# Kernel tuning notes

Measured on AMD Instinct MI355X. Metric: run time of the kernel, lower is better.

## Reference

```python
import jax, jax.numpy as jnp
import numpy as np
import math

B, N, D, O, H = 2, 3072, 64, 64, 4

def setup_inputs() -> dict:
    key = jax.random.key(0)
    ks = jax.random.split(key, 8)
    x = jax.random.normal(ks[0], (B, N, D), dtype=jnp.float32)
    edge_index = jax.random.randint(ks[1], (B, N, N), 0, 2, dtype=jnp.int32)
    s = 1.0 / math.sqrt(D)
    Wv = jax.random.uniform(ks[2], (H, D, O), jnp.float32, -s, s)
    bv = jax.random.uniform(ks[3], (H, O), jnp.float32, -s, s)
    Wq = jax.random.uniform(ks[4], (H, D, O), jnp.float32, -s, s)
    bq = jax.random.uniform(ks[5], (H, O), jnp.float32, -s, s)
    Wk = jax.random.uniform(ks[6], (H, D, O), jnp.float32, -s, s)
    bk = jax.random.uniform(ks[7], (H, O), jnp.float32, -s, s)
    return {"x": x, "edge_index": edge_index, "Wv": Wv, "bv": bv,
            "Wq": Wq, "bq": bq, "Wk": Wk, "bk": bk}

def reference(x, edge_index, Wv, bv, Wq, bq, Wk, bk):
    # x: [B,N,D]; edge_index: dense {0,1} adjacency [B,N,N]
    dk = jnp.asarray(math.sqrt(x.shape[-1]), x.dtype)
    v = jnp.einsum('bnd,hdo->bhno', x, Wv) + bv[None, :, None, :]
    q = jnp.einsum('bnd,hdo->bhno', x, Wq) + bq[None, :, None, :]
    k = jnp.einsum('bnd,hdo->bhno', x, Wk) + bk[None, :, None, :]
    scores = jnp.einsum('bhno,bhmo->bhnm', q, k) / dk        # [B,H,N,N]
    scores = jax.nn.leaky_relu(scores, 0.2)
    mask = (-1e10) * (1.0 - edge_index.astype(scores.dtype))  # [B,N,N]
    scores = scores + mask[:, None, :, :]
    prop = jax.nn.softmax(scores, axis=-1)
    # dropout on v omitted (inference mode: identity)
    feats = jnp.einsum('bhnm,bhmo->bhno', prop, v)            # [B,H,N,O]
    out = jnp.mean(feats, axis=1)                             # [B,N,O]
    return jax.nn.leaky_relu(out, 0.2)
```

## Files before the change

### kernel.cpp

```cpp
#include <hip/hip_runtime.h>
#include <hip/hip_bf16.h>
#include <cstdint>

#define Bc 2
#define Nc 3072
#define Hc 4
#define NW32 96
#define TILEB 8192
#define KSC 4
#define TPS (NW32/KSC)

typedef __bf16    bf16x8 __attribute__((ext_vector_type(8)));
typedef _Float16  f16x8  __attribute__((ext_vector_type(8)));
typedef _Float16  f16x4  __attribute__((ext_vector_type(4)));
typedef float     f32x16 __attribute__((ext_vector_type(16)));

#define QSCALE 0.18033688f

static __device__ __forceinline__ f32x16 mfma32bf(bf16x8 a, bf16x8 b, f32x16 c) {
    return __builtin_amdgcn_mfma_f32_32x32x16_bf16(a, b, c, 0, 0, 0);
}
static __device__ __forceinline__ f32x16 mfma32h(f16x8 a, f16x8 b, f32x16 c) {
    return __builtin_amdgcn_mfma_f32_32x32x16_f16(a, b, c, 0, 0, 0);
}
static __device__ __forceinline__ uint32_t pkrtz(float lo, float hi) {
    uint32_t w;
    asm("v_cvt_pkrtz_f16_f32 %0, %1, %2" : "=v"(w) : "v"(lo), "v"(hi));
    return w;
}

static __device__ __forceinline__ void softmax_pack(const f32x16& sc, uint32_t mwh,
                                                    uint32_t W8[8])
{
    #pragma unroll
    for (int i = 0; i < 8; ++i) {
        const int bp0 = (2*i & 3) + 8*(2*i >> 2);
        float s0 = sc[2*i], s1 = sc[2*i + 1];
        float a0 = fmaxf(s0, 0.2f*s0);
        float a1 = fmaxf(s1, 0.2f*s1);
        float e0, e1;
        asm("v_exp_f32 %0, %1" : "=v"(e0) : "v"(a0));
        asm("v_exp_f32 %0, %1" : "=v"(e1) : "v"(a1));
        uint32_t pk = pkrtz(e0, e1);
        uint32_t m0 = (uint32_t)__builtin_amdgcn_sbfe((int)mwh, bp0, 1);
        uint32_t m1 = (uint32_t)__builtin_amdgcn_sbfe((int)mwh, bp0 + 1, 1);
        uint32_t sel = (m0 & 0x0000ffffu) | (m1 & 0xffff0000u);
        W8[i] = pk & sel;
    }
}

static __device__ __forceinline__ void assemble_pa(uint32_t W8[8], f16x8& pa0, f16x8& pa1)
{
    uint32_t a0 = W8[0], a2 = W8[2], a1 = W8[1], a3 = W8[3];
    uint32_t b0 = W8[4], b2 = W8[6], b1 = W8[5], b3 = W8[7];
    asm("v_permlane32_swap_b32 %0, %1" : "+v"(a0), "+v"(a2));
    asm("v_permlane32_swap_b32 %0, %1" : "+v"(a1), "+v"(a3));
    asm("v_permlane32_swap_b32 %0, %1" : "+v"(b0), "+v"(b2));
    asm("v_permlane32_swap_b32 %0, %1" : "+v"(b1), "+v"(b3));
    union { uint32_t u[4]; f16x8 v; } u0, u1;
    u0.u[0] = a0; u0.u[1] = a1; u0.u[2] = a2; u0.u[3] = a3;
    u1.u[0] = b0; u1.u[1] = b1; u1.u[2] = b2; u1.u[3] = b3;
    pa0 = u0.v; pa1 = u1.v;
}

static __device__ __forceinline__ void load_subtile(const char* gt, int hi, int l31,
                                                    f16x8 (&K)[4], f16x8 (&V)[4])
{
    #pragma unroll
    for (int kk = 0; kk < 4; ++kk)
        K[kk] = *(const f16x8*)(gt + ((kk*2 + hi) << 9) + (l31 << 4));
    #pragma unroll
    for (int i = 0; i < 4; ++i) {
        const int kkp = i >> 1, ot = i & 1;
        V[i] = *(const f16x8*)(gt + 4096 + ((kkp*2 + hi) << 10) + ((ot*32 + l31) << 4));
    }
}

static __device__ __forceinline__ void compute_subtile(
    const f16x8 (&K)[4], const f16x8 (&V)[4], uint32_t mw, int hi,
    const f16x8 (&qf)[4], const f32x16& fzero, const f16x8& ones,
    f32x16& acc0, f32x16& acc1, f32x16& acc2)
{
    f32x16 sc;
    __builtin_amdgcn_s_setprio(1);
    sc = mfma32h(K[0], qf[0], fzero);
    sc = mfma32h(K[1], qf[1], sc);
    sc = mfma32h(K[2], qf[2], sc);
    sc = mfma32h(K[3], qf[3], sc);
    __builtin_amdgcn_s_setprio(0);

    uint32_t W8[8];
    softmax_pack(sc, mw >> (hi*4), W8);
    f16x8 pa0, pa1;
    assemble_pa(W8, pa0, pa1);

    __builtin_amdgcn_s_setprio(1);
    acc2 = mfma32h(pa0, ones, acc2);
    acc2 = mfma32h(pa1, ones, acc2);
    acc0 = mfma32h(pa0, V[0], acc0);
    acc1 = mfma32h(pa0, V[1], acc1);
    acc0 = mfma32h(pa1, V[2], acc0);
    acc1 = mfma32h(pa1, V[3], acc1);
    __builtin_amdgcn_s_setprio(0);
}

__global__ void preppack_kernel(const float* __restrict__ Wq, const float* __restrict__ Wk,
                                const float* __restrict__ Wv,
                                const float* __restrict__ bq, const float* __restrict__ bk,
                                const float* __restrict__ bv,
                                const int* __restrict__ edge,
                                __bf16* __restrict__ Wbh, __bf16* __restrict__ Wbl,
                                float* __restrict__ Bs, uint32_t* __restrict__ pmT)
{
    if (blockIdx.x < 192) {
        int i = blockIdx.x*256 + threadIdx.x;
        int d = i & 63, o = (i >> 6) & 63, h = (i >> 12) & 3, p = i >> 14;
        const float* W = (p == 0) ? Wq : (p == 1) ? Wk : Wv;
        float scale = (p == 0) ? QSCALE : 1.0f;
        float val = W[(h*64 + d)*64 + o] * scale;
        int idx = (((p*Hc + h)*64 + o) << 6) + d;
        __bf16 hi = (__bf16)val;
        Wbh[idx] = hi;
        Wbl[idx] = (__bf16)(val - (float)hi);
        if (i < 3*Hc*64) {
            int pp = i / (Hc*64), rest = i % (Hc*64);
            const float* B = (pp == 0) ? bq : (pp == 1) ? bk : bv;
            Bs[i] = B[rest] * ((pp == 0) ? QSCALE : 1.0f);
        }
    } else {
        int gw = (blockIdx.x - 192)*4 + (threadIdx.x >> 6);
        int lane = threadIdx.x & 63;
        int ng = gw % 48; gw /= 48;
        int w  = gw % NW32; gw /= NW32;
        int b  = gw;
        int n = ng*64 + lane;
        const uint4* ep = (const uint4*)(edge + ((size_t)b*Nc + n)*Nc + w*32);
        uint32_t word = 0;
        #pragma unroll
        for (int i = 0; i < 8; ++i) {
            uint4 e = ep[i];
            word |= (e.x ? 1u : 0u) << (4*i);
            word |= (e.y ? 1u : 0u) << (4*i + 1);
            word |= (e.z ? 1u : 0u) << (4*i + 2);
            word |= (e.w ? 1u : 0u) << (4*i + 3);
        }
        pmT[((size_t)b*NW32 + w)*Nc + n] = word;
    }
}

__global__ __launch_bounds__(256) void qkv_mfma(
    const float* __restrict__ x,
    const __bf16* __restrict__ Wbh, const __bf16* __restrict__ Wbl,
    const float* __restrict__ Bs,
    _Float16* __restrict__ Qf, _Float16* __restrict__ Kf,
    _Float16* __restrict__ KVimg)
{
    const int lane = threadIdx.x & 63, w = threadIdx.x >> 6;
    const int l31 = lane & 31, hi = lane >> 5;
    int t = blockIdx.x;
    int nt = t % 48; t /= 48;
    int b  = t & 1;  t >>= 1;
    int p  = t % 3;
    int h  = t / 3;
    const int r0 = (w >> 1)*32, c0 = (w & 1)*32, n0 = nt*64;

    bf16x8 xh[4], xl[4], wh[4], wl[4];
    #pragma unroll
    for (int kk = 0; kk < 4; ++kk) {
        size_t xoff = (((size_t)(b*Nc + n0 + r0 + l31)) << 6) + kk*16 + hi*8;
        float4 f0 = *(const float4*)(x + xoff);
        float4 f1 = *(const float4*)(x + xoff + 4);
        float xs[8] = {f0.x, f0.y, f0.z, f0.w, f1.x, f1.y, f1.z, f1.w};
        #pragma unroll
        for (int j = 0; j < 8; ++j) {
            __bf16 hh = (__bf16)xs[j];
            xh[kk][j] = hh;
            xl[kk][j] = (__bf16)(xs[j] - (float)hh);
        }
        size_t woff = (((size_t)((p*Hc + h)*64 + c0 + l31)) << 6) + kk*16 + hi*8;
        wh[kk] = *(const bf16x8*)(Wbh + woff);
        wl[kk] = *(const bf16x8*)(Wbl + woff);
    }
    float bias = Bs[(p*Hc + h)*64 + c0 + l31];
    f32x16 acc;
    #pragma unroll
    for (int i = 0; i < 16; ++i) acc[i] = bias;
    #pragma unroll
    for (int kk = 0; kk < 4; ++kk) {
        acc = mfma32bf(xh[kk], wh[kk], acc);
        acc = mfma32bf(xl[kk], wh[kk], acc);
        acc = mfma32bf(xh[kk], wl[kk], acc);
    }
    const int bh = b*Hc + h;
    if (p < 2) {
        _Float16* dst = (p == 0) ? Qf : Kf;
        #pragma unroll
        for (int r = 0; r < 16; ++r) {
            int row = (r & 3) + 8*(r >> 2) + 4*hi;
            size_t idx = (((size_t)bh*Nc + n0 + r0 + row) << 6) + c0 + l31;
            dst[idx] = (_Float16)acc[r];
        }
    } else {
        const int t_img = (n0 + r0) >> 5;
        char* img = (char*)KVimg + (size_t)(bh*96 + t_img)*TILEB;
        #pragma unroll
        for (int grp = 0; grp < 2; ++grp) {
            uint32_t wH[4];
            #pragma unroll
            for (int j = 0; j < 4; ++j)
                wH[j] = pkrtz(acc[grp*8 + 2*j], acc[grp*8 + 2*j + 1]);
            asm("v_permlane32_swap_b32 %0, %1" : "+v"(wH[0]), "+v"(wH[2]));
            asm("v_permlane32_swap_b32 %0, %1" : "+v"(wH[1]), "+v"(wH[3]));
            const int kb = grp*2 + hi;
            const int o  = c0 + l31;
            uint4 gh = {wH[0], wH[1], wH[2], wH[3]};
            *(uint4*)(img + 4096 + ((kb*64 + o) << 4)) = gh;
        }
    }
}

__global__ void imgk_kernel(const _Float16* __restrict__ Kf, _Float16* __restrict__ KVimg)
{
    const int t = blockIdx.x % 96, bh = blockIdx.x / 96;
    char* img = (char*)KVimg + (size_t)(bh*96 + t)*TILEB;
    int dc = threadIdx.x & 7, key = threadIdx.x >> 3;
    size_t src = (((size_t)bh*Nc + t*32 + key) << 6) + dc*8;
    *(uint4*)(img + (dc*32 + key)*16) = *(const uint4*)(Kf + src);
}

__global__ __launch_bounds__(256, 3) void attn_mfma(
    const _Float16* __restrict__ Qf,
    const _Float16* __restrict__ KVimg, const uint32_t* __restrict__ pmT,
    _Float16* __restrict__ PAh, float* __restrict__ PL)
{
    const int lane = threadIdx.x & 63, w = threadIdx.x >> 6;
    const int l31 = lane & 31, hi = lane >> 5;
    int gb = blockIdx.x;
    const int bh = gb & 7; gb >>= 3;
    const int qt = gb % 24;
    const int ks = gb / 24;
    const int b = bh >> 2;
    const int qrow0 = qt*128 + w*32;
    const int t0 = ks*TPS;

    const uint32_t* pmp = pmT + ((size_t)b*NW32 + t0)*Nc + qrow0 + l31;
    const char* gt = (const char*)KVimg + (size_t)(bh*96 + t0)*TILEB;

    f16x8 qf[4];
    #pragma unroll
    for (int kk = 0; kk < 4; ++kk) {
        size_t qoff = (((size_t)bh*Nc + qrow0 + l31) << 6) + kk*16 + hi*8;
        qf[kk] = *(const f16x8*)(Qf + qoff);
    }
    f32x16 fzero;
    #pragma unroll
    for (int i = 0; i < 16; ++i) fzero[i] = 0.f;
    f16x8 ones;
    #pragma unroll
    for (int j = 0; j < 8; ++j) ones[j] = (_Float16)1.0f;

    f32x16 acc0 = fzero, acc1 = fzero, acc2 = fzero;

    f16x8 KA[4], VA[4], KB[4], VB[4];
    uint32_t mwA, mwB;
    load_subtile(gt, hi, l31, KA, VA);
    mwA = pmp[0];

    #pragma unroll 1
    for (int j = 0; j < TPS/2; ++j) {
        load_subtile(gt + (size_t)(2*j + 1)*TILEB, hi, l31, KB, VB);
        mwB = pmp[(size_t)(2*j + 1)*Nc];
        compute_subtile(KA, VA, mwA, hi, qf, fzero, ones, acc0, acc1, acc2);
        const int tn = (2*j + 2 < TPS) ? (2*j + 2) : 0;
        load_subtile(gt + (size_t)tn*TILEB, hi, l31, KA, VA);
        mwA = pmp[(size_t)tn*Nc];
        compute_subtile(KB, VB, mwB, hi, qf, fzero, ones, acc0, acc1, acc2);
    }

    _Float16* po = PAh + (((size_t)(bh*KSC + ks)*Nc + qrow0) << 6);
    #pragma unroll
    for (int r = 0; r < 16; ++r) {
        int row = (r & 3) + 8*(r >> 2) + 4*hi;
        po[((size_t)row << 6) + l31]      = (_Float16)acc0[r];
        po[((size_t)row << 6) + 32 + l31] = (_Float16)acc1[r];
    }
    if (l31 == 0) {
        float* pl = PL + (size_t)(bh*KSC + ks)*Nc + qrow0;
        #pragma unroll
        for (int r = 0; r < 16; ++r)
            pl[(r & 3) + 8*(r >> 2) + 4*hi] = acc2[r];
    }
}

__global__ void merge_kernel(const _Float16* __restrict__ PAh,
                             const float* __restrict__ PL, float* __restrict__ out)
{
    int gid = blockIdx.x*256 + threadIdx.x;
    int og = (gid & 15) << 2;
    int bn = gid >> 4;
    int n  = bn % Nc;
    int b  = bn / Nc;
    float f0 = 0.f, f1 = 0.f, f2 = 0.f, f3 = 0.f;
    for (int h = 0; h < Hc; ++h) {
        int bh = b*Hc + h;
        float A0 = 0.f, A1 = 0.f, A2 = 0.f, A3 = 0.f, L = 0.f;
        for (int ks = 0; ks < KSC; ++ks) {
            size_t base = ((size_t)(bh*KSC + ks)*Nc + n);
            f16x4 a = *(const f16x4*)(PAh + (base << 6) + og);
            A0 += (float)a[0]; A1 += (float)a[1];
            A2 += (float)a[2]; A3 += (float)a[3];
            L  += PL[base];
        }
        float invL = 1.0f / L;
        f0 += A0*invL; f1 += A1*invL; f2 += A2*invL; f3 += A3*invL;
    }
    float4 r;
    r.x = f0*0.25f; r.y = f1*0.25f; r.z = f2*0.25f; r.w = f3*0.25f;
    r.x = fmaxf(r.x, 0.f) + 0.2f*fminf(r.x, 0.f);
    r.y = fmaxf(r.y, 0.f) + 0.2f*fminf(r.y, 0.f);
    r.z = fmaxf(r.z, 0.f) + 0.2f*fminf(r.z, 0.f);
    r.w = fmaxf(r.w, 0.f) + 0.2f*fminf(r.w, 0.f);
    *(float4*)(out + ((size_t)bn << 6) + og) = r;
}

extern "C" void kernel_launch(void* const* d_in, const int* in_sizes, int n_in,
                              void* d_out, int out_size, void* d_ws, size_t ws_size,
                              hipStream_t stream)
{
    const float* x    = (const float*)d_in[0];
    const int*   edge = (const int*)d_in[1];
    const float* Wv   = (const float*)d_in[2];
    const float* bv   = (const float*)d_in[3];
    const float* Wq   = (const float*)d_in[4];
    const float* bq   = (const float*)d_in[5];
    const float* Wk   = (const float*)d_in[6];
    const float* bk   = (const float*)d_in[7];
    float* out = (float*)d_out;

    const size_t PROJ = (size_t)Bc*Hc*Nc*64;
    char* p = (char*)d_ws;
    __bf16* Wbh = (__bf16*)p;     p += 49152*2;
    __bf16* Wbl = (__bf16*)p;     p += 49152*2;
    float*  Bs  = (float*)p;      p += 4096;
    _Float16* Qf = (_Float16*)p;  p += PROJ*2;
    _Float16* Kf = (_Float16*)p;  p += PROJ*2;
    _Float16* KVimg = (_Float16*)p; p += (size_t)Bc*Hc*96*TILEB;
    uint32_t* pmT = (uint32_t*)p; p += (size_t)Bc*NW32*Nc*4;
    _Float16* PAh = (_Float16*)p; p += (size_t)Bc*Hc*KSC*Nc*64*2;
    float* PL = (float*)p;

    hipLaunchKernelGGL(preppack_kernel, dim3(192 + Bc*NW32*48/4), dim3(256), 0, stream,
                       Wq, Wk, Wv, bq, bk, bv, edge, Wbh, Wbl, Bs, pmT);
    hipLaunchKernelGGL(qkv_mfma,    dim3(1152), dim3(256), 0, stream,
                       x, Wbh, Wbl, Bs, Qf, Kf, KVimg);
    hipLaunchKernelGGL(imgk_kernel, dim3(Bc*Hc*96), dim3(256), 0, stream, Kf, KVimg);
    hipLaunchKernelGGL(attn_mfma,   dim3(8*KSC*24), dim3(256), 0, stream,
                       Qf, KVimg, pmT, PAh, PL);
    hipLaunchKernelGGL(merge_kernel, dim3((Bc*Nc*16)/256), dim3(256), 0, stream,
                       PAh, PL, out);
}
```

Baseline: 72.33 us.

## Replace row-sum MFMAs with VALU dot2 sums and interleave two subtile score passes

The softmax denominator is no longer computed with two extra MFMAs against a ones vector. Each lane now accumulates its masked fp16 exponentials with v_dot2_f32_f16, and a single cross-half shuffle finishes the per-query sum. The main loop is also restructured: both subtiles' QK score MFMAs issue back to back, and loads for the next pair are issued after each subtile's PV MFMAs, with both buffers prefetched before the loop. This cuts MFMA work per tile, but adds VALU instructions and raises register pressure from holding two score accumulators.

```diff
diff --git a/kernel.cpp b/kernel.cpp
--- a/kernel.cpp
+++ b/kernel.cpp
@@ -30,7 +30,8 @@
 }
 
 static __device__ __forceinline__ void softmax_pack(const f32x16& sc, uint32_t mwh,
-                                                    uint32_t W8[8])
+                                                    uint32_t W8[8], float& lsum,
+                                                    uint32_t ones32)
 {
     #pragma unroll
     for (int i = 0; i < 8; ++i) {
@@ -45,7 +46,9 @@
         uint32_t m0 = (uint32_t)__builtin_amdgcn_sbfe((int)mwh, bp0, 1);
         uint32_t m1 = (uint32_t)__builtin_amdgcn_sbfe((int)mwh, bp0 + 1, 1);
         uint32_t sel = (m0 & 0x0000ffffu) | (m1 & 0xffff0000u);
-        W8[i] = pk & sel;
+        uint32_t wv = pk & sel;
+        W8[i] = wv;
+        asm("v_dot2_f32_f16 %0, %1, %2, %0" : "+v"(lsum) : "v"(wv), "v"(ones32));
     }
 }
 
@@ -74,34 +77,6 @@
         const int kkp = i >> 1, ot = i & 1;
         V[i] = *(const f16x8*)(gt + 4096 + ((kkp*2 + hi) << 10) + ((ot*32 + l31) << 4));
     }
-}
-
-static __device__ __forceinline__ void compute_subtile(
-    const f16x8 (&K)[4], const f16x8 (&V)[4], uint32_t mw, int hi,
-    const f16x8 (&qf)[4], const f32x16& fzero, const f16x8& ones,
-    f32x16& acc0, f32x16& acc1, f32x16& acc2)
-{
-    f32x16 sc;
-    __builtin_amdgcn_s_setprio(1);
-    sc = mfma32h(K[0], qf[0], fzero);
-    sc = mfma32h(K[1], qf[1], sc);
-    sc = mfma32h(K[2], qf[2], sc);
-    sc = mfma32h(K[3], qf[3], sc);
-    __builtin_amdgcn_s_setprio(0);
-
-    uint32_t W8[8];
-    softmax_pack(sc, mw >> (hi*4), W8);
-    f16x8 pa0, pa1;
-    assemble_pa(W8, pa0, pa1);
-
-    __builtin_amdgcn_s_setprio(1);
-    acc2 = mfma32h(pa0, ones, acc2);
-    acc2 = mfma32h(pa1, ones, acc2);
-    acc0 = mfma32h(pa0, V[0], acc0);
-    acc1 = mfma32h(pa0, V[1], acc1);
-    acc0 = mfma32h(pa1, V[2], acc0);
-    acc1 = mfma32h(pa1, V[3], acc1);
-    __builtin_amdgcn_s_setprio(0);
 }
 
 __global__ void preppack_kernel(const float* __restrict__ Wq, const float* __restrict__ Wk,
@@ -255,28 +230,67 @@
     f32x16 fzero;
     #pragma unroll
     for (int i = 0; i < 16; ++i) fzero[i] = 0.f;
-    f16x8 ones;
-    #pragma unroll
-    for (int j = 0; j < 8; ++j) ones[j] = (_Float16)1.0f;
-
-    f32x16 acc0 = fzero, acc1 = fzero, acc2 = fzero;
+    const uint32_t ones32 = 0x3C003C00u;
+
+    f32x16 acc0 = fzero, acc1 = fzero;
+    float lsum = 0.f;
 
     f16x8 KA[4], VA[4], KB[4], VB[4];
-    uint32_t mwA, mwB;
     load_subtile(gt, hi, l31, KA, VA);
-    mwA = pmp[0];
+    load_subtile(gt + TILEB, hi, l31, KB, VB);
+    uint32_t mwA = pmp[0];
+    uint32_t mwB = pmp[Nc];
 
     #pragma unroll 1
     for (int j = 0; j < TPS/2; ++j) {
-        load_subtile(gt + (size_t)(2*j + 1)*TILEB, hi, l31, KB, VB);
-        mwB = pmp[(size_t)(2*j + 1)*Nc];
-        compute_subtile(KA, VA, mwA, hi, qf, fzero, ones, acc0, acc1, acc2);
-        const int tn = (2*j + 2 < TPS) ? (2*j + 2) : 0;
-        load_subtile(gt + (size_t)tn*TILEB, hi, l31, KA, VA);
-        mwA = pmp[(size_t)tn*Nc];
-        compute_subtile(KB, VB, mwB, hi, qf, fzero, ones, acc0, acc1, acc2);
-    }
-
+        f32x16 scA, scB;
+        __builtin_amdgcn_s_setprio(1);
+        scA = mfma32h(KA[0], qf[0], fzero);
+        scA = mfma32h(KA[1], qf[1], scA);
+        scA = mfma32h(KA[2], qf[2], scA);
+        scA = mfma32h(KA[3], qf[3], scA);
+        scB = mfma32h(KB[0], qf[0], fzero);
+        scB = mfma32h(KB[1], qf[1], scB);
+        scB = mfma32h(KB[2], qf[2], scB);
+        scB = mfma32h(KB[3], qf[3], scB);
+        __builtin_amdgcn_s_setprio(0);
+
+        {
+            uint32_t W8[8];
+            softmax_pack(scA, mwA >> (hi*4), W8, lsum, ones32);
+            f16x8 pa0, pa1;
+            assemble_pa(W8, pa0, pa1);
+            __builtin_amdgcn_s_setprio(1);
+            acc0 = mfma32h(pa0, VA[0], acc0);
+            acc1 = mfma32h(pa0, VA[1], acc1);
+            acc0 = mfma32h(pa1, VA[2], acc0);
+            acc1 = mfma32h(pa1, VA[3], acc1);
+            __builtin_amdgcn_s_setprio(0);
+        }
+        const int tA = (2*j + 2 < TPS) ? (2*j + 2) : 0;
+        load_subtile(gt + (size_t)tA*TILEB, hi, l31, KA, VA);
+        uint32_t nmwA = pmp[(size_t)tA*Nc];
+
+        {
+            uint32_t W8[8];
+            softmax_pack(scB, mwB >> (hi*4), W8, lsum, ones32);
+            f16x8 pa0, pa1;
+            assemble_pa(W8, pa0, pa1);
+            __builtin_amdgcn_s_setprio(1);
+            acc0 = mfma32h(pa0, VB[0], acc0);
+            acc1 = mfma32h(pa0, VB[1], acc1);
+            acc0 = mfma32h(pa1, VB[2], acc0);
+            acc1 = mfma32h(pa1, VB[3], acc1);
+            __builtin_amdgcn_s_setprio(0);
+        }
+        const int tB = (2*j + 3 < TPS) ? (2*j + 3) : 1;
+        load_subtile(gt + (size_t)tB*TILEB, hi, l31, KB, VB);
+        uint32_t nmwB = pmp[(size_t)tB*Nc];
+
+        mwA = nmwA; mwB = nmwB;
+    }
+
+    lsum += __shfl_xor(lsum, 32);
     _Float16* po = PAh + (((size_t)(bh*KSC + ks)*Nc + qrow0) << 6);
     #pragma unroll
     for (int r = 0; r < 16; ++r) {
@@ -284,12 +298,8 @@
         po[((size_t)row << 6) + l31]      = (_Float16)acc0[r];
         po[((size_t)row << 6) + 32 + l31] = (_Float16)acc1[r];
     }
-    if (l31 == 0) {
-        float* pl = PL + (size_t)(bh*KSC + ks)*Nc + qrow0;
-        #pragma unroll
-        for (int r = 0; r < 16; ++r)
-            pl[(r & 3) + 8*(r >> 2) + 4*hi] = acc2[r];
-    }
+    if (lane < 32)
+        PL[(size_t)(bh*KSC + ks)*Nc + qrow0 + l31] = lsum;
 }
 
 __global__ void merge_kernel(const _Float16* __restrict__ PAh,
```

Result: no change. 73.35 us (+1.4%).
